# Performance work log

Measured on AMD Instinct MI355X. Metric: run time of the kernel, lower is better.

Reference implementation:

```python
import jax, jax.numpy as jnp
import numpy as np

N, D = 8192, 128
EPS = 1e-6  # torch F.pairwise_distance default eps


def _pe(d, s=3, t=2):
    # 1/d^s - 1/d^t
    return 1.0 / (d ** s) - 1.0 / (d ** t)


def setup_inputs() -> dict:
    key = jax.random.key(0)
    x = jax.random.normal(key, (N, D), dtype=jnp.float32)
    return {"x": x}


def reference(x):
    n = x.shape[0]
    # loss0: distance of each row to the origin; torch pairwise_distance adds eps to the diff
    d0 = jnp.sqrt(jnp.sum((x + EPS) ** 2, axis=-1))  # [N]
    loss0 = jnp.mean(jnp.clip(_pe(d0), -1.5, 1000.0))

    # pdist: condensed upper-triangular pairwise Euclidean distances (no eps)
    sq = jnp.sum(x * x, axis=-1)                      # [N]
    d2 = sq[:, None] + sq[None, :] - 2.0 * (x @ x.T)  # [N, N]
    mask = jnp.triu(jnp.ones((n, n), dtype=bool), k=1)
    # keep masked entries at 1.0 so sqrt/pe stay finite
    d2 = jnp.where(mask, jnp.maximum(d2, 0.0), 1.0)
    d = jnp.sqrt(d2)
    vals = jnp.clip(_pe(d), -1.5, 1000.0)
    cnt = n * (n - 1) // 2
    loss = jnp.sum(jnp.where(mask, vals, 0.0)) / cnt
    return loss0 + loss
```

## Files before the change

kernel.cpp:

```cpp
#include <hip/hip_runtime.h>
#include <hip/hip_bf16.h>


#define NROWS 8192
#define DDIM  128
#define TILE  128
#define TTILES (NROWS / TILE)
#define NTRI  (TTILES * (TTILES + 1) / 2)
#define NBLKP 512
#define FEPS  1e-6f

typedef float f32x4 __attribute__((ext_vector_type(4)));
typedef short s16x8 __attribute__((ext_vector_type(8)));

__global__ __launch_bounds__(256) void convert_kernel(
        const float* __restrict__ x, unsigned int* __restrict__ xb_u32,
        float* __restrict__ sq, float* __restrict__ p0) {
    int tid = threadIdx.x;
    int wave = tid >> 6, lane = tid & 63;
    int row = blockIdx.x * 4 + wave;

    float2 v = *(const float2*)(x + (size_t)row * DDIM + lane * 2);
    float s = v.x * v.x + v.y * v.y;
    float ex = v.x + FEPS, ey = v.y + FEPS;
    float e = ex * ex + ey * ey;

    __hip_bfloat16 b0 = __float2bfloat16(v.x);
    __hip_bfloat16 b1 = __float2bfloat16(v.y);
    unsigned short u0 = *reinterpret_cast<unsigned short*>(&b0);
    unsigned short u1 = *reinterpret_cast<unsigned short*>(&b1);
    xb_u32[(size_t)row * (DDIM / 2) + lane] = (unsigned)u0 | ((unsigned)u1 << 16);

    #pragma unroll
    for (int off = 32; off; off >>= 1) {
        s += __shfl_down(s, off);
        e += __shfl_down(e, off);
    }

    __shared__ float red[4];
    if (lane == 0) {
        sq[row] = s;
        float r = rsqrtf(e);
        float r2 = r * r;
        red[wave] = fminf(fmaxf(r2 * r - r2, -1.5f), 1000.0f);
    }
    __syncthreads();
    if (tid == 0) p0[blockIdx.x] = red[0] + red[1] + red[2] + red[3];
}

__device__ __forceinline__ int tri_off(int i) {
    return i * TTILES - ((i * (i - 1)) >> 1);
}

__device__ __forceinline__ void decode_tile(int t, int& I, int& J) {
    float T2 = 2.0f * TTILES + 1.0f;
    int i = (int)((T2 - sqrtf(T2 * T2 - 8.0f * (float)t)) * 0.5f);
    while (tri_off(i + 1) <= t) ++i;
    while (tri_off(i) > t) --i;
    I = i;
    J = i + (t - tri_off(i));
}

__device__ __forceinline__ void stage_tile(const char* __restrict__ g,
                                           char* lds, int tid) {
    int l = tid & 63, w = tid >> 6;
    uint4 v[4];
    #pragma unroll
    for (int p = 0; p < 4; ++p)
        v[p] = *(const uint4*)(g + ((w * 4 + p) * 64 + l) * 16);
    #pragma unroll
    for (int p = 0; p < 4; ++p) {
        int chunk = (w * 4 + p) * 64 + l;
        int row = chunk >> 4, c = chunk & 15;
        *(uint4*)(lds + row * 256 + ((c * 16) ^ ((row & 7) << 4))) = v[p];
    }
}

__global__ __launch_bounds__(512, 4) void pair_kernel(
        const __hip_bfloat16* __restrict__ xb_h,
        const float* __restrict__ sq, float* __restrict__ pp) {
    const char* xb = (const char*)xb_h;
    __shared__ char smem[65536];
    char* ldsA = smem;
    char* ldsB = smem + 32768;

    int b = blockIdx.x;
    int t0, cnt;
    if (b < 32) { t0 = b * 5; cnt = 5; }
    else        { t0 = 32 + b * 4; cnt = 4; }

    int I, J;
    decode_tile(t0, I, J);

    int tid = threadIdx.x;
    int wave = tid >> 6, lane = tid & 63;
    int wR = (wave >> 2) * 64;
    int wC = (wave & 3) * 32;
    int lcol = lane & 15;
    int lrow = lane >> 4;

    float lsum = 0.0f;
    int curI = -1;

    for (int k = 0; k < cnt; ++k) {
        if (I != curI) { stage_tile(xb + (size_t)I * TILE * 256, ldsA, tid); curI = I; }
        bool diag = (I == J);
        if (!diag) stage_tile(xb + (size_t)J * TILE * 256, ldsB, tid);
        __syncthreads();
        const char* bufB = diag ? ldsA : ldsB;

        f32x4 acc[4][2];
        #pragma unroll
        for (int r = 0; r < 4; ++r)
            #pragma unroll
            for (int c = 0; c < 2; ++c) acc[r][c] = (f32x4){0.f, 0.f, 0.f, 0.f};

        #pragma unroll
        for (int ks = 0; ks < 4; ++ks) {
            int kb = ks * 64 + lrow * 16;
            s16x8 a[4], bb[2];
            #pragma unroll
            for (int r = 0; r < 4; ++r) {
                int row = wR + r * 16 + lcol;
                a[r] = *(const s16x8*)(ldsA + row * 256 + (kb ^ ((row & 7) << 4)));
            }
            #pragma unroll
            for (int c = 0; c < 2; ++c) {
                int row = wC + c * 16 + lcol;
                bb[c] = *(const s16x8*)(bufB + row * 256 + (kb ^ ((row & 7) << 4)));
            }
            #pragma unroll
            for (int r = 0; r < 4; ++r)
                #pragma unroll
                for (int c = 0; c < 2; ++c)
                    acc[r][c] = __builtin_amdgcn_mfma_f32_16x16x32_bf16(
                        a[r], bb[c], acc[r][c], 0, 0, 0);
        }

        int ibase = I * TILE + wR + lrow * 4;
        int jbase = J * TILE + wC + lcol;
        float sqj[2];
        #pragma unroll
        for (int c = 0; c < 2; ++c) sqj[c] = sq[jbase + c * 16];

        if (!diag) {
            #pragma unroll
            for (int r = 0; r < 4; ++r)
                #pragma unroll
                for (int u = 0; u < 4; ++u) {
                    float si = sq[ibase + r * 16 + u];
                    #pragma unroll
                    for (int c = 0; c < 2; ++c) {
                        float d2 = si + sqj[c] - 2.0f * acc[r][c][u];
                        float rv = rsqrtf(d2);
                        float r2 = rv * rv;
                        lsum += r2 * rv - r2;
                    }
                }
        } else {
            int il0 = wR + lrow * 4;
            int jl0 = wC + lcol;
            #pragma unroll
            for (int r = 0; r < 4; ++r)
                #pragma unroll
                for (int u = 0; u < 4; ++u) {
                    int il = il0 + r * 16 + u;
                    float si = sq[ibase + r * 16 + u];
                    #pragma unroll
                    for (int c = 0; c < 2; ++c) {
                        if (jl0 + c * 16 > il) {
                            float d2 = fmaxf(si + sqj[c] - 2.0f * acc[r][c][u], 1e-30f);
                            float rv = rsqrtf(d2);
                            float r2 = rv * rv;
                            lsum += fminf(r2 * rv - r2, 1000.0f);
                        }
                    }
                }
        }
        __syncthreads();

        ++J;
        if (J == TTILES) { ++I; J = I; }
    }

    #pragma unroll
    for (int off = 32; off; off >>= 1) lsum += __shfl_down(lsum, off);
    __shared__ float red[8];
    if (lane == 0) red[wave] = lsum;
    __syncthreads();
    if (tid == 0) {
        float t = 0.f;
        #pragma unroll
        for (int w = 0; w < 8; ++w) t += red[w];
        pp[blockIdx.x] = t;
    }
}

__global__ __launch_bounds__(1024) void reduce_kernel(
        const float* __restrict__ p0, int n0,
        const float* __restrict__ pp, int np, float* __restrict__ out) {
    int tid = threadIdx.x;
    double s0 = 0.0, sp = 0.0;
    for (int i = tid; i < n0; i += 1024) s0 += (double)p0[i];
    for (int i = tid; i < np; i += 1024) sp += (double)pp[i];
    __shared__ double sh0[1024], shp[1024];
    sh0[tid] = s0; shp[tid] = sp;
    __syncthreads();
    for (int s = 512; s; s >>= 1) {
        if (tid < s) { sh0[tid] += sh0[tid + s]; shp[tid] += shp[tid + s]; }
        __syncthreads();
    }
    if (tid == 0) {
        double cnt = (double)NROWS * (double)(NROWS - 1) * 0.5;
        out[0] = (float)(sh0[0] / (double)NROWS + shp[0] / cnt);
    }
}

extern "C" void kernel_launch(void* const* d_in, const int* in_sizes, int n_in,
                              void* d_out, int out_size, void* d_ws, size_t ws_size,
                              hipStream_t stream) {
    const float* x = (const float*)d_in[0];
    char* ws = (char*)d_ws;
    const size_t OFF_SQ = 2097152;
    const size_t OFF_P0 = OFF_SQ + 32768;
    const size_t OFF_PP = OFF_P0 + 8192;
    if (ws_size < OFF_PP + NBLKP * sizeof(float)) return;

    unsigned int* xb_u32 = (unsigned int*)ws;
    __hip_bfloat16* xb = (__hip_bfloat16*)ws;
    float* sq = (float*)(ws + OFF_SQ);
    float* p0 = (float*)(ws + OFF_P0);
    float* pp = (float*)(ws + OFF_PP);

    convert_kernel<<<NROWS / 4, 256, 0, stream>>>(x, xb_u32, sq, p0);
    pair_kernel<<<NBLKP, 512, 0, stream>>>(xb, sq, pp);
    reduce_kernel<<<1, 1024, 0, stream>>>(p0, NROWS / 4, pp, NBLKP, (float*)d_out);
}
```

Before: 33.46 us.

## Switch Gram matrix to FP8 MFMA, rebalance tiles, fuse final reduction

```diff
diff --git a/kernel.cpp b/kernel.cpp
--- a/kernel.cpp
+++ b/kernel.cpp
@@ -5,31 +5,31 @@
 #define NROWS 8192
 #define DDIM  128
 #define TILE  128
+#define RB    128
 #define TTILES (NROWS / TILE)
 #define NTRI  (TTILES * (TTILES + 1) / 2)
-#define NBLKP 512
+#define NBLKP 696
 #define FEPS  1e-6f
 
 typedef float f32x4 __attribute__((ext_vector_type(4)));
-typedef short s16x8 __attribute__((ext_vector_type(8)));
+typedef long long i64;
 
 __global__ __launch_bounds__(256) void convert_kernel(
-        const float* __restrict__ x, unsigned int* __restrict__ xb_u32,
-        float* __restrict__ sq, float* __restrict__ p0) {
+        const float* __restrict__ x, unsigned short* __restrict__ xf8_u16,
+        float* __restrict__ sq, float* __restrict__ p0, int* __restrict__ counter) {
     int tid = threadIdx.x;
     int wave = tid >> 6, lane = tid & 63;
     int row = blockIdx.x * 4 + wave;
+
+    if (blockIdx.x == 0 && tid == 0) *counter = 0;
 
     float2 v = *(const float2*)(x + (size_t)row * DDIM + lane * 2);
     float s = v.x * v.x + v.y * v.y;
     float ex = v.x + FEPS, ey = v.y + FEPS;
     float e = ex * ex + ey * ey;
 
-    __hip_bfloat16 b0 = __float2bfloat16(v.x);
-    __hip_bfloat16 b1 = __float2bfloat16(v.y);
-    unsigned short u0 = *reinterpret_cast<unsigned short*>(&b0);
-    unsigned short u1 = *reinterpret_cast<unsigned short*>(&b1);
-    xb_u32[(size_t)row * (DDIM / 2) + lane] = (unsigned)u0 | ((unsigned)u1 << 16);
+    int packed = __builtin_amdgcn_cvt_pk_fp8_f32(v.x, v.y, 0, false);
+    xf8_u16[(size_t)row * 64 + lane] = (unsigned short)(packed & 0xFFFF);
 
     #pragma unroll
     for (int off = 32; off; off >>= 1) {
@@ -52,45 +52,43 @@
     return i * TTILES - ((i * (i - 1)) >> 1);
 }
 
-__device__ __forceinline__ void decode_tile(int t, int& I, int& J) {
-    float T2 = 2.0f * TTILES + 1.0f;
-    int i = (int)((T2 - sqrtf(T2 * T2 - 8.0f * (float)t)) * 0.5f);
-    while (tri_off(i + 1) <= t) ++i;
-    while (tri_off(i) > t) --i;
-    I = i;
-    J = i + (t - tri_off(i));
-}
-
 __device__ __forceinline__ void stage_tile(const char* __restrict__ g,
                                            char* lds, int tid) {
-    int l = tid & 63, w = tid >> 6;
-    uint4 v[4];
-    #pragma unroll
-    for (int p = 0; p < 4; ++p)
-        v[p] = *(const uint4*)(g + ((w * 4 + p) * 64 + l) * 16);
-    #pragma unroll
-    for (int p = 0; p < 4; ++p) {
-        int chunk = (w * 4 + p) * 64 + l;
-        int row = chunk >> 4, c = chunk & 15;
-        *(uint4*)(lds + row * 256 + ((c * 16) ^ ((row & 7) << 4))) = v[p];
-    }
-}
-
-__global__ __launch_bounds__(512, 4) void pair_kernel(
-        const __hip_bfloat16* __restrict__ xb_h,
-        const float* __restrict__ sq, float* __restrict__ pp) {
-    const char* xb = (const char*)xb_h;
-    __shared__ char smem[65536];
+    uint4 v[2];
+    #pragma unroll
+    for (int p = 0; p < 2; ++p)
+        v[p] = *(const uint4*)(g + (p * 512 + tid) * 16);
+    #pragma unroll
+    for (int p = 0; p < 2; ++p) {
+        int n = p * 512 + tid;
+        int row = n >> 3, c = n & 7;
+        *(uint4*)(lds + row * RB + ((c * 16) ^ ((row & 7) << 4))) = v[p];
+    }
+}
+
+__global__ __launch_bounds__(512, 6) void pair_kernel(
+        const unsigned short* __restrict__ xf8_u16,
+        const float* __restrict__ sq, float* __restrict__ pp,
+        const float* __restrict__ p0, int* __restrict__ counter,
+        float* __restrict__ out) {
+    const char* xb = (const char*)xf8_u16;
+    __shared__ char smem[32768];
     char* ldsA = smem;
-    char* ldsB = smem + 32768;
+    char* ldsB = smem + 16384;
 
     int b = blockIdx.x;
     int t0, cnt;
-    if (b < 32) { t0 = b * 5; cnt = 5; }
-    else        { t0 = 32 + b * 4; cnt = 4; }
-
-    int I, J;
-    decode_tile(t0, I, J);
+    if (b < 688) { t0 = b * 3; cnt = 3; }
+    else         { t0 = 2064 + (b - 688) * 2; cnt = 2; }
+
+    int I = 0;
+    {
+        float T2 = 2.0f * TTILES + 1.0f;
+        I = (int)((T2 - sqrtf(T2 * T2 - 8.0f * (float)t0)) * 0.5f);
+        while (tri_off(I + 1) <= t0) ++I;
+        while (tri_off(I) > t0) --I;
+    }
+    int J = I + (t0 - tri_off(I));
 
     int tid = threadIdx.x;
     int wave = tid >> 6, lane = tid & 63;
@@ -103,9 +101,9 @@
     int curI = -1;
 
     for (int k = 0; k < cnt; ++k) {
-        if (I != curI) { stage_tile(xb + (size_t)I * TILE * 256, ldsA, tid); curI = I; }
+        if (I != curI) { stage_tile(xb + (size_t)I * TILE * RB, ldsA, tid); curI = I; }
         bool diag = (I == J);
-        if (!diag) stage_tile(xb + (size_t)J * TILE * 256, ldsB, tid);
+        if (!diag) stage_tile(xb + (size_t)J * TILE * RB, ldsB, tid);
         __syncthreads();
         const char* bufB = diag ? ldsA : ldsB;
 
@@ -117,23 +115,23 @@
 
         #pragma unroll
         for (int ks = 0; ks < 4; ++ks) {
-            int kb = ks * 64 + lrow * 16;
-            s16x8 a[4], bb[2];
+            int koff = ks * 32 + lrow * 8;
+            i64 a[4], bb[2];
             #pragma unroll
             for (int r = 0; r < 4; ++r) {
                 int row = wR + r * 16 + lcol;
-                a[r] = *(const s16x8*)(ldsA + row * 256 + (kb ^ ((row & 7) << 4)));
+                a[r] = *(const i64*)(ldsA + row * RB + (koff ^ ((row & 7) << 4)));
             }
             #pragma unroll
             for (int c = 0; c < 2; ++c) {
                 int row = wC + c * 16 + lcol;
-                bb[c] = *(const s16x8*)(bufB + row * 256 + (kb ^ ((row & 7) << 4)));
+                bb[c] = *(const i64*)(bufB + row * RB + (koff ^ ((row & 7) << 4)));
             }
             #pragma unroll
             for (int r = 0; r < 4; ++r)
                 #pragma unroll
                 for (int c = 0; c < 2; ++c)
-                    acc[r][c] = __builtin_amdgcn_mfma_f32_16x16x32_bf16(
+                    acc[r][c] = __builtin_amdgcn_mfma_f32_16x16x32_fp8_fp8(
                         a[r], bb[c], acc[r][c], 0, 0, 0);
         }
 
@@ -186,6 +184,7 @@
     #pragma unroll
     for (int off = 32; off; off >>= 1) lsum += __shfl_down(lsum, off);
     __shared__ float red[8];
+    __shared__ int amLast;
     if (lane == 0) red[wave] = lsum;
     __syncthreads();
     if (tid == 0) {
@@ -193,26 +192,25 @@
         #pragma unroll
         for (int w = 0; w < 8; ++w) t += red[w];
         pp[blockIdx.x] = t;
-    }
-}
-
-__global__ __launch_bounds__(1024) void reduce_kernel(
-        const float* __restrict__ p0, int n0,
-        const float* __restrict__ pp, int np, float* __restrict__ out) {
-    int tid = threadIdx.x;
-    double s0 = 0.0, sp = 0.0;
-    for (int i = tid; i < n0; i += 1024) s0 += (double)p0[i];
-    for (int i = tid; i < np; i += 1024) sp += (double)pp[i];
-    __shared__ double sh0[1024], shp[1024];
-    sh0[tid] = s0; shp[tid] = sp;
+        __threadfence();
+        amLast = (atomicAdd(counter, 1) == NBLKP - 1);
+    }
     __syncthreads();
-    for (int s = 512; s; s >>= 1) {
-        if (tid < s) { sh0[tid] += sh0[tid + s]; shp[tid] += shp[tid + s]; }
+
+    if (amLast) {
+        __threadfence();
+        double cnt2 = (double)NROWS * (double)(NROWS - 1) * 0.5;
+        double s = 0.0;
+        for (int i = tid; i < NBLKP; i += 512) s += (double)pp[i] / cnt2;
+        for (int i = tid; i < NROWS / 4; i += 512) s += (double)p0[i] / (double)NROWS;
+        double* sh = (double*)smem;
+        sh[tid] = s;
         __syncthreads();
-    }
-    if (tid == 0) {
-        double cnt = (double)NROWS * (double)(NROWS - 1) * 0.5;
-        out[0] = (float)(sh0[0] / (double)NROWS + shp[0] / cnt);
+        for (int st = 256; st; st >>= 1) {
+            if (tid < st) sh[tid] += sh[tid + st];
+            __syncthreads();
+        }
+        if (tid == 0) out[0] = (float)sh[0];
     }
 }
 
@@ -221,18 +219,18 @@
                               hipStream_t stream) {
     const float* x = (const float*)d_in[0];
     char* ws = (char*)d_ws;
-    const size_t OFF_SQ = 2097152;
-    const size_t OFF_P0 = OFF_SQ + 32768;
-    const size_t OFF_PP = OFF_P0 + 8192;
-    if (ws_size < OFF_PP + NBLKP * sizeof(float)) return;
-
-    unsigned int* xb_u32 = (unsigned int*)ws;
-    __hip_bfloat16* xb = (__hip_bfloat16*)ws;
+    const size_t OFF_SQ  = 1048576;
+    const size_t OFF_P0  = OFF_SQ + 32768;
+    const size_t OFF_PP  = OFF_P0 + 8192;
+    const size_t OFF_CNT = OFF_PP + ((NBLKP * 4 + 255) & ~255);
+    if (ws_size < OFF_CNT + 256) return;
+
+    unsigned short* xf8 = (unsigned short*)ws;
     float* sq = (float*)(ws + OFF_SQ);
     float* p0 = (float*)(ws + OFF_P0);
     float* pp = (float*)(ws + OFF_PP);
-
-    convert_kernel<<<NROWS / 4, 256, 0, stream>>>(x, xb_u32, sq, p0);
-    pair_kernel<<<NBLKP, 512, 0, stream>>>(xb, sq, pp);
-    reduce_kernel<<<1, 1024, 0, stream>>>(p0, NROWS / 4, pp, NBLKP, (float*)d_out);
-}
+    int* counter = (int*)(ws + OFF_CNT);
+
+    convert_kernel<<<NROWS / 4, 256, 0, stream>>>(x, xf8, sq, p0, counter);
+    pair_kernel<<<NBLKP, 512, 0, stream>>>(xf8, sq, pp, p0, counter, (float*)d_out);
+}
```

After: 43.79 us. 30.9% more time.
